# Kernel tuning notes

Measured on AMD Instinct MI355X. Metric: run time of the kernel, lower is better.

## Reference

```python
import jax, jax.numpy as jnp
import numpy as np

D_MODEL = 1024
NUM_HEADS = 16
HEAD_DIM = D_MODEL // NUM_HEADS  # 64


def setup_inputs() -> dict:
    key = jax.random.key(0)
    ks = jax.random.split(key, 9)
    s = 1.0 / np.sqrt(D_MODEL)
    return {
        "x": jax.random.normal(ks[0], (2, 2048, D_MODEL), dtype=jnp.float32),
        "Wq": jax.random.normal(ks[1], (D_MODEL, D_MODEL), dtype=jnp.float32) * s,
        "bq": jnp.zeros((D_MODEL,), dtype=jnp.float32),
        "Wk": jax.random.normal(ks[2], (D_MODEL, HEAD_DIM), dtype=jnp.float32) * s,
        "bk": jnp.zeros((HEAD_DIM,), dtype=jnp.float32),
        "Wv": jax.random.normal(ks[3], (D_MODEL, HEAD_DIM), dtype=jnp.float32) * s,
        "bv": jnp.zeros((HEAD_DIM,), dtype=jnp.float32),
        "Wo": jax.random.normal(ks[4], (D_MODEL, D_MODEL), dtype=jnp.float32) * s,
        "bo": jnp.zeros((D_MODEL,), dtype=jnp.float32),
    }


def reference(x, Wq, bq, Wk, bk, Wv, bv, Wo, bo):
    B, S, D = x.shape
    H, hd = NUM_HEADS, HEAD_DIM
    # Projections: Q has H heads, K/V a single shared head (MQA).
    Q = (x @ Wq + bq).reshape(B, S, H, hd).transpose(0, 2, 1, 3)  # [B,H,S,hd]
    K = x @ Wk + bk  # [B,S,hd]
    V = x @ Wv + bv  # [B,S,hd]
    # Shared-K/V attention: broadcast K across heads instead of expand().
    scores = jnp.einsum("bhqd,bkd->bhqk", Q, K) / np.sqrt(hd)  # [B,H,S,S]
    attn = jax.nn.softmax(scores, axis=-1)
    attended = jnp.einsum("bhqk,bkd->bhqd", attn, V)  # [B,H,S,hd]
    attended = attended.transpose(0, 2, 1, 3).reshape(B, S, D)
    return attended @ Wo + bo
```

## Files before the change

kernel.cpp:

```cpp
#include <hip/hip_runtime.h>
#include <hip/hip_bf16.h>

#define D_MODEL 1024
#define NHEADS  16
#define HD      64
#define BATCH   2
#define SEQ     2048
#define MROWS   4096
#define NQKV    1152
#define NSPLIT  2

typedef short  short4v __attribute__((ext_vector_type(4)));
typedef short  short8  __attribute__((ext_vector_type(8)));
typedef float  floatx4 __attribute__((ext_vector_type(4)));
typedef unsigned uint4v __attribute__((ext_vector_type(4)));

__device__ inline short f2bf(float f) {
  unsigned u = __builtin_bit_cast(unsigned, f);
  u = (u + 0x7FFF + ((u >> 16) & 1)) >> 16;
  return (short)u;
}

__device__ inline unsigned pack_trunc(float lo, float hi) {
  return __builtin_amdgcn_perm(__builtin_bit_cast(unsigned, hi),
                               __builtin_bit_cast(unsigned, lo), 0x07060302u);
}

__device__ inline void async_copy16(const short* g, short* l) {
  __builtin_amdgcn_global_load_lds(
      (const __attribute__((address_space(1))) unsigned int*)g,
      (__attribute__((address_space(3))) unsigned int*)l, 16, 0, 0);
}

__global__ __launch_bounds__(256)
void prep_kernel(const float* __restrict__ x,  const float* __restrict__ Wq,
                 const float* __restrict__ Wk, const float* __restrict__ Wv,
                 const float* __restrict__ Wo, const float* __restrict__ bq,
                 const float* __restrict__ bk, const float* __restrict__ bv,
                 short* __restrict__ xb, short* __restrict__ Wqkv_t,
                 short* __restrict__ Wo_t, float* __restrict__ bqkv) {
  const int id = blockIdx.x;
  const int t  = threadIdx.x;
  if (id < 544) {
    __shared__ short Ts[64 * 72];
    const float* src; short* dst; int N, off, tile;
    if (id < 256)      { src = Wq; dst = Wqkv_t; N = 1024; off = 0;    tile = id; }
    else if (id < 272) { src = Wk; dst = Wqkv_t; N = 64;   off = 1024; tile = id - 256; }
    else if (id < 288) { src = Wv; dst = Wqkv_t; N = 64;   off = 1088; tile = id - 272; }
    else               { src = Wo; dst = Wo_t;   N = 1024; off = 0;    tile = id - 288; }
    const int k0 = (N == 1024) ? (tile & 15) * 64 : tile * 64;
    const int n0 = (N == 1024) ? (tile >> 4) * 64 : 0;
    {
      const int r = t >> 2, c = (t & 3) * 16;
      const float* s = src + (size_t)(k0 + r) * N + n0 + c;
#pragma unroll
      for (int j = 0; j < 16; j += 4) {
        float4 v = *reinterpret_cast<const float4*>(s + j);
        Ts[r * 72 + c + j + 0] = f2bf(v.x); Ts[r * 72 + c + j + 1] = f2bf(v.y);
        Ts[r * 72 + c + j + 2] = f2bf(v.z); Ts[r * 72 + c + j + 3] = f2bf(v.w);
      }
    }
    __syncthreads();
    {
      const int n = t >> 2, kc = (t & 3) * 16;
      short8 o0, o1;
#pragma unroll
      for (int j = 0; j < 8; ++j) o0[j] = Ts[(kc + j) * 72 + n];
#pragma unroll
      for (int j = 0; j < 8; ++j) o1[j] = Ts[(kc + 8 + j) * 72 + n];
      short* d = dst + (size_t)(off + n0 + n) * 1024 + k0 + kc;
      *reinterpret_cast<short8*>(d)     = o0;
      *reinterpret_cast<short8*>(d + 8) = o1;
    }
  } else if (id < 549) {
    const int i = (id - 544) * 256 + t;
    if (i < 1024)      bqkv[i] = bq[i];
    else if (i < 1088) bqkv[i] = bk[i - 1024];
    else if (i < 1152) bqkv[i] = bv[i - 1088];
  } else {
    const int i = ((id - 549) * 256 + t) * 8;
    if (i < MROWS * D_MODEL) {
      float4 a = *reinterpret_cast<const float4*>(x + i);
      float4 b = *reinterpret_cast<const float4*>(x + i + 4);
      short8 o;
      o[0] = f2bf(a.x); o[1] = f2bf(a.y); o[2] = f2bf(a.z); o[3] = f2bf(a.w);
      o[4] = f2bf(b.x); o[5] = f2bf(b.y); o[6] = f2bf(b.z); o[7] = f2bf(b.w);
      *reinterpret_cast<short8*>(xb + i) = o;
    }
  }
}

template<bool OUT_BF16, int SCALE_N, bool VT_FUSE>
__global__ __launch_bounds__(256)
void gemm_mfma_bt(const short* __restrict__ A, const short* __restrict__ Bt,
                  const float* __restrict__ bias, void* __restrict__ Cout,
                  short* __restrict__ Vtg, int M, int N, int K) {
  __shared__ short As[2][128 * 64];
  __shared__ short Bs[2][64 * 64];
  const int t    = threadIdx.x;
  const int w    = t >> 6;
  const int lane = t & 63;
  const int quad = lane >> 4;
  const int l16  = lane & 15;
  const int bm   = blockIdx.x * 128;
  const int bn   = blockIdx.y * 64;
  const int wm   = (w >> 1) * 64;
  const int wn   = (w & 1) * 32;

  const int srow = t >> 3;
  const int cc   = ((t & 7) ^ (srow & 7)) * 8;
  const short* gA = A  + (size_t)(bm + srow) * K + cc;
  const short* gB = Bt + (size_t)(bn + srow) * K + cc;

  floatx4 acc[4][2];
#pragma unroll
  for (int i = 0; i < 4; ++i)
#pragma unroll
    for (int j = 0; j < 2; ++j) acc[i][j] = (floatx4){0.f, 0.f, 0.f, 0.f};

  const int xr = l16 & 7;

  async_copy16(gA, &As[0][t * 8]);
  async_copy16(gA + (size_t)32 * K, &As[0][t * 8 + 2048]);
  async_copy16(gA + (size_t)64 * K, &As[0][t * 8 + 4096]);
  async_copy16(gA + (size_t)96 * K, &As[0][t * 8 + 6144]);
  async_copy16(gB, &Bs[0][t * 8]);
  async_copy16(gB + (size_t)32 * K, &Bs[0][t * 8 + 2048]);

  int cur = 0;
  for (int k0 = 0; k0 < K; k0 += 64) {
    asm volatile("s_waitcnt vmcnt(0)" ::: "memory");
    __builtin_amdgcn_s_barrier();
    __builtin_amdgcn_sched_barrier(0);

    if (k0 + 64 < K) {
      const int nb = cur ^ 1;
      const int kn = k0 + 64;
      async_copy16(gA + kn, &As[nb][t * 8]);
      async_copy16(gA + (size_t)32 * K + kn, &As[nb][t * 8 + 2048]);
      async_copy16(gA + (size_t)64 * K + kn, &As[nb][t * 8 + 4096]);
      async_copy16(gA + (size_t)96 * K + kn, &As[nb][t * 8 + 6144]);
      async_copy16(gB + kn, &Bs[nb][t * 8]);
      async_copy16(gB + (size_t)32 * K + kn, &Bs[nb][t * 8 + 2048]);
    }
    __builtin_amdgcn_sched_barrier(0);

    const short* Ac = As[cur];
    const short* Bc = Bs[cur];
    short8 fa0[4], fa1[4], fb0[2], fb1[2];
#pragma unroll
    for (int mi = 0; mi < 4; ++mi) {
      const int row = wm + mi * 16 + l16;
      fa0[mi] = *reinterpret_cast<const short8*>(&Ac[row * 64 + (quad ^ xr) * 8]);
      fa1[mi] = *reinterpret_cast<const short8*>(&Ac[row * 64 + ((4 + quad) ^ xr) * 8]);
    }
#pragma unroll
    for (int ni = 0; ni < 2; ++ni) {
      const int row = wn + ni * 16 + l16;
      fb0[ni] = *reinterpret_cast<const short8*>(&Bc[row * 64 + (quad ^ xr) * 8]);
      fb1[ni] = *reinterpret_cast<const short8*>(&Bc[row * 64 + ((4 + quad) ^ xr) * 8]);
    }
#pragma unroll
    for (int mi = 0; mi < 4; ++mi)
#pragma unroll
      for (int ni = 0; ni < 2; ++ni) {
        acc[mi][ni] = __builtin_amdgcn_mfma_f32_16x16x32_bf16(fa0[mi], fb0[ni], acc[mi][ni], 0, 0, 0);
        acc[mi][ni] = __builtin_amdgcn_mfma_f32_16x16x32_bf16(fa1[mi], fb1[ni], acc[mi][ni], 0, 0, 0);
      }
    cur ^= 1;
  }

#pragma unroll
  for (int ni = 0; ni < 2; ++ni) {
    const int col = bn + wn + ni * 16 + l16;
    const float bs = bias[col];
    const float sc = (col < SCALE_N) ? 0.18033688f : 1.0f;
#pragma unroll
    for (int mi = 0; mi < 4; ++mi) {
      const int row = bm + wm + mi * 16 + quad * 4;
      short4v vt4;
#pragma unroll
      for (int r = 0; r < 4; ++r) {
        const float v = (acc[mi][ni][r] + bs) * sc;
        if (OUT_BF16) {
          const short bv16 = f2bf(v);
          ((short*)Cout)[(size_t)(row + r) * N + col] = bv16;
          if (VT_FUSE) vt4[r] = bv16;
        } else {
          ((float*)Cout)[(size_t)(row + r) * N + col] = v;
        }
      }
      if (VT_FUSE && col >= 1088) {
        const int d = col - 1088;
        const int b = row >> 11, s = row & 2047;
        *reinterpret_cast<short4v*>(&Vtg[(size_t)(b * 64 + d) * SEQ + s]) = vt4;
      }
    }
  }
}

__global__ __launch_bounds__(256, 3)
void mqa_flash_bf16(const short* __restrict__ QKV, const short* __restrict__ Vtg,
                    _Float16* __restrict__ Opart, float* __restrict__ lpart) {
  const int bh    = blockIdx.y;
  const int b     = bh >> 4;
  const int h     = bh & 15;
  const int s0    = blockIdx.x * 128;
  const int split = blockIdx.z;
  const int t     = threadIdx.x;
  const int w     = t >> 6;
  const int lane  = t & 63;
  const int quad  = lane >> 4;
  const int l16   = lane & 15;

  __shared__ short KVs[16384];

  short8 aq[2][2];
#pragma unroll
  for (int st = 0; st < 2; ++st) {
    const short* qrow = &QKV[(size_t)(b * SEQ + s0 + w * 32 + st * 16 + l16) * NQKV + h * HD];
    aq[st][0] = *reinterpret_cast<const short8*>(qrow + quad * 8);
    aq[st][1] = *reinterpret_cast<const short8*>(qrow + 32 + quad * 8);
  }

  floatx4 oacc[2][4];
  floatx4 lacc[2];
#pragma unroll
  for (int st = 0; st < 2; ++st) {
    lacc[st] = (floatx4){0.f, 0.f, 0.f, 0.f};
#pragma unroll
    for (int dg = 0; dg < 4; ++dg) oacc[st][dg] = (floatx4){0.f, 0.f, 0.f, 0.f};
  }

  short8 ones;
#pragma unroll
  for (int j = 0; j < 8; ++j) ones[j] = (short)0x3F80;

  const int srow  = t >> 3;
  const int cc    = ((t & 7) ^ (srow & 7)) * 8;
  const int krow  = ((srow >> 4) & 1) * 4 + ((srow >> 2) & 3) * 8 + (srow & 3);
  const int kbase = split * (SEQ / NSPLIT);
  const short* gK = QKV + (size_t)(b * SEQ + kbase + krow) * NQKV + 1024 + cc;
  const short* gV = Vtg + (size_t)(b * 64 + srow) * SEQ + kbase + cc;
  short* lK = KVs + w * 512;
  short* lV = KVs + 4096 + w * 512;

  const int xr = l16 & 7;

  async_copy16(gK, lK);
  async_copy16(gK + (size_t)32 * NQKV, lK + 2048);
  async_copy16(gV, lV);
  async_copy16(gV + (size_t)32 * SEQ, lV + 2048);
  gK += (size_t)64 * NQKV;
  gV += 64;

  const int NT = (SEQ / NSPLIT) / 64;
  int cur = 0;

  for (int it = 0; it < NT; ++it) {
    asm volatile("s_waitcnt vmcnt(0)" ::: "memory");
    __builtin_amdgcn_s_barrier();
    __builtin_amdgcn_sched_barrier(0);

    if (it + 1 < NT) {
      const int nb = (cur ^ 1) * 8192;
      async_copy16(gK, lK + nb);
      async_copy16(gK + (size_t)32 * NQKV, lK + nb + 2048);
      async_copy16(gV, lV + nb);
      async_copy16(gV + (size_t)32 * SEQ, lV + nb + 2048);
      gK += (size_t)64 * NQKV;
      gV += 64;
    }
    __builtin_amdgcn_sched_barrier(0);

    const short* Ks = KVs + cur * 8192;
    const short* Vt = Ks + 4096;

    short8 kb[4][2], vb[4][2];
#pragma unroll
    for (int kg = 0; kg < 4; ++kg) {
      kb[kg][0] = *reinterpret_cast<const short8*>(&Ks[(kg * 16 + l16) * 64 + (quad ^ xr) * 8]);
      kb[kg][1] = *reinterpret_cast<const short8*>(&Ks[(kg * 16 + l16) * 64 + ((4 + quad) ^ xr) * 8]);
    }
#pragma unroll
    for (int dg = 0; dg < 4; ++dg) {
      vb[dg][0] = *reinterpret_cast<const short8*>(&Vt[(dg * 16 + l16) * 64 + (quad ^ xr) * 8]);
      vb[dg][1] = *reinterpret_cast<const short8*>(&Vt[(dg * 16 + l16) * 64 + ((4 + quad) ^ xr) * 8]);
    }

#pragma unroll
    for (int st = 0; st < 2; ++st) {
      floatx4 s4[4];
#pragma unroll
      for (int kg = 0; kg < 4; ++kg) {
        s4[kg] = (floatx4){0.f, 0.f, 0.f, 0.f};
        s4[kg] = __builtin_amdgcn_mfma_f32_16x16x32_bf16(kb[kg][0], aq[st][0], s4[kg], 0, 0, 0);
        s4[kg] = __builtin_amdgcn_mfma_f32_16x16x32_bf16(kb[kg][1], aq[st][1], s4[kg], 0, 0, 0);
      }
      unsigned pk[8];
#pragma unroll
      for (int kg = 0; kg < 4; ++kg) {
        const float p0 = __builtin_exp2f(s4[kg][0]);
        const float p1 = __builtin_exp2f(s4[kg][1]);
        const float p2 = __builtin_exp2f(s4[kg][2]);
        const float p3 = __builtin_exp2f(s4[kg][3]);
        pk[kg * 2 + 0] = pack_trunc(p0, p1);
        pk[kg * 2 + 1] = pack_trunc(p2, p3);
      }
      const uint4v u0 = (uint4v){pk[0], pk[1], pk[2], pk[3]};
      const uint4v u1 = (uint4v){pk[4], pk[5], pk[6], pk[7]};
      const short8 ap0 = __builtin_bit_cast(short8, u0);
      const short8 ap1 = __builtin_bit_cast(short8, u1);

      __builtin_amdgcn_s_setprio(1);
      lacc[st] = __builtin_amdgcn_mfma_f32_16x16x32_bf16(ap0, ones, lacc[st], 0, 0, 0);
      lacc[st] = __builtin_amdgcn_mfma_f32_16x16x32_bf16(ap1, ones, lacc[st], 0, 0, 0);
#pragma unroll
      for (int dg = 0; dg < 4; ++dg) {
        oacc[st][dg] = __builtin_amdgcn_mfma_f32_16x16x32_bf16(ap0, vb[dg][0], oacc[st][dg], 0, 0, 0);
        oacc[st][dg] = __builtin_amdgcn_mfma_f32_16x16x32_bf16(ap1, vb[dg][1], oacc[st][dg], 0, 0, 0);
      }
      __builtin_amdgcn_s_setprio(0);
    }
    cur ^= 1;
  }

#pragma unroll
  for (int st = 0; st < 2; ++st) {
#pragma unroll
    for (int rg = 0; rg < 4; ++rg) {
      const int qg = s0 + w * 32 + st * 16 + quad * 4 + rg;
      _Float16* dst = Opart + ((size_t)(split * 32 + bh) * SEQ + qg) * 64 + l16;
#pragma unroll
      for (int dg = 0; dg < 4; ++dg) dst[dg * 16] = (_Float16)oacc[st][dg][rg];
      if (l16 == 0) lpart[(size_t)(split * 32 + bh) * SEQ + qg] = lacc[st][rg];
    }
  }
}

__global__ __launch_bounds__(256)
void combine_kernel(const _Float16* __restrict__ Opart, const float* __restrict__ lpart,
                    short* __restrict__ Att) {
  const int idx = blockIdx.x * 256 + threadIdx.x;
  const int r   = idx >> 3;
  const int d0  = (idx & 7) * 8;
  float l = 0.f;
  float o[8] = {0.f,0.f,0.f,0.f,0.f,0.f,0.f,0.f};
#pragma unroll
  for (int s = 0; s < NSPLIT; ++s) {
    const _Float16* op = Opart + ((size_t)(s * 32 * SEQ) + r) * 64 + d0;
    l += lpart[(size_t)s * 32 * SEQ + r];
#pragma unroll
    for (int j = 0; j < 8; ++j) o[j] += (float)op[j];
  }
  const float inv = 1.0f / l;
  short8 ov;
#pragma unroll
  for (int j = 0; j < 8; ++j) ov[j] = f2bf(o[j] * inv);
  const int bhh = r >> 11, q = r & 2047;
  const int bb = bhh >> 4, hh = bhh & 15;
  *reinterpret_cast<short8*>(&Att[(size_t)(bb * SEQ + q) * D_MODEL + hh * HD + d0]) = ov;
}

extern "C" void kernel_launch(void* const* d_in, const int* in_sizes, int n_in,
                              void* d_out, int out_size, void* d_ws, size_t ws_size,
                              hipStream_t stream) {
  const float* x  = (const float*)d_in[0];
  const float* Wq = (const float*)d_in[1];
  const float* bq = (const float*)d_in[2];
  const float* Wk = (const float*)d_in[3];
  const float* bk = (const float*)d_in[4];
  const float* Wv = (const float*)d_in[5];
  const float* bv = (const float*)d_in[6];
  const float* Wo = (const float*)d_in[7];
  const float* bo = (const float*)d_in[8];
  float* out = (float*)d_out;

  short* Wqkv_t = (short*)d_ws;
  short* Wo_t   = Wqkv_t + (size_t)NQKV * D_MODEL;
  short* xb     = Wo_t + (size_t)D_MODEL * D_MODEL;
  short* QKV    = xb + (size_t)MROWS * D_MODEL;
  short* Att    = QKV + (size_t)MROWS * NQKV;
  short* Vtg    = Att + (size_t)MROWS * D_MODEL;
  float* bqkv   = (float*)(Vtg + (size_t)BATCH * HD * SEQ);
  float* lpart  = bqkv + 1152;
  _Float16* Opart = (_Float16*)(lpart + (size_t)NSPLIT * 32 * SEQ);

  prep_kernel<<<2597, 256, 0, stream>>>(x, Wq, Wk, Wv, Wo, bq, bk, bv,
                                        xb, Wqkv_t, Wo_t, bqkv);

  gemm_mfma_bt<true, 1024, true><<<dim3(MROWS / 128, NQKV / 64), 256, 0, stream>>>(
      xb, Wqkv_t, bqkv, QKV, Vtg, MROWS, NQKV, D_MODEL);

  mqa_flash_bf16<<<dim3(SEQ / 128, BATCH * NHEADS, NSPLIT), 256, 0, stream>>>(
      QKV, Vtg, Opart, lpart);

  combine_kernel<<<2048, 256, 0, stream>>>(Opart, lpart, Att);

  gemm_mfma_bt<false, 0, false><<<dim3(MROWS / 128, D_MODEL / 64), 256, 0, stream>>>(
      Att, Wo_t, bo, out, nullptr, MROWS, D_MODEL, D_MODEL);
}
```

Measured before the change: 171.3 us.

## Drop split-K attention and combine kernel; use 128-key tiles with fused normalization

Removes the two-way key split and the separate combine kernel. Each flash block now walks the full sequence and normalizes by the row sum before writing bf16 straight into the attention buffer. K/V staging is widened to 128-key tiles, so LDS use doubles and the occupancy hint drops from 3 to 2 blocks. This avoids the fp16 partial-output round trip and one launch, at the cost of half as many blocks (512) in the grid and longer per-block loops.

```diff
diff --git a/kernel.cpp b/kernel.cpp
--- a/kernel.cpp
+++ b/kernel.cpp
@@ -8,7 +8,6 @@
 #define SEQ     2048
 #define MROWS   4096
 #define NQKV    1152
-#define NSPLIT  2
 
 typedef short  short4v __attribute__((ext_vector_type(4)));
 typedef short  short8  __attribute__((ext_vector_type(8)));
@@ -199,21 +198,20 @@
   }
 }
 
-__global__ __launch_bounds__(256, 3)
+__global__ __launch_bounds__(256, 2)
 void mqa_flash_bf16(const short* __restrict__ QKV, const short* __restrict__ Vtg,
-                    _Float16* __restrict__ Opart, float* __restrict__ lpart) {
-  const int bh    = blockIdx.y;
-  const int b     = bh >> 4;
-  const int h     = bh & 15;
-  const int s0    = blockIdx.x * 128;
-  const int split = blockIdx.z;
-  const int t     = threadIdx.x;
-  const int w     = t >> 6;
-  const int lane  = t & 63;
-  const int quad  = lane >> 4;
-  const int l16   = lane & 15;
-
-  __shared__ short KVs[16384];
+                    short* __restrict__ Att) {
+  const int bh   = blockIdx.y;
+  const int b    = bh >> 4;
+  const int h    = bh & 15;
+  const int s0   = blockIdx.x * 128;
+  const int t    = threadIdx.x;
+  const int w    = t >> 6;
+  const int lane = t & 63;
+  const int quad = lane >> 4;
+  const int l16  = lane & 15;
+
+  __shared__ short KVs[2][16384];
 
   short8 aq[2][2];
 #pragma unroll
@@ -236,25 +234,35 @@
 #pragma unroll
   for (int j = 0; j < 8; ++j) ones[j] = (short)0x3F80;
 
-  const int srow  = t >> 3;
-  const int cc    = ((t & 7) ^ (srow & 7)) * 8;
-  const int krow  = ((srow >> 4) & 1) * 4 + ((srow >> 2) & 3) * 8 + (srow & 3);
-  const int kbase = split * (SEQ / NSPLIT);
-  const short* gK = QKV + (size_t)(b * SEQ + kbase + krow) * NQKV + 1024 + cc;
-  const short* gV = Vtg + (size_t)(b * 64 + srow) * SEQ + kbase + cc;
-  short* lK = KVs + w * 512;
-  short* lV = KVs + 4096 + w * 512;
+  const int srow = t >> 3;
+  const int ccK  = ((t & 7) ^ (srow & 7)) * 8;
+  const int krow = ((srow >> 4) & 1) * 4 + ((srow >> 2) & 3) * 8 + (srow & 3);
+  const short* gK = QKV + (size_t)(b * SEQ + krow) * NQKV + 1024 + ccK;
+  const int vrow = t >> 4;
+  const int ccV  = ((t & 15) ^ (vrow & 7)) * 8;
+  const short* gV = Vtg + (size_t)(b * 64 + vrow) * SEQ + ccV;
 
   const int xr = l16 & 7;
 
-  async_copy16(gK, lK);
-  async_copy16(gK + (size_t)32 * NQKV, lK + 2048);
-  async_copy16(gV, lV);
-  async_copy16(gV + (size_t)32 * SEQ, lV + 2048);
-  gK += (size_t)64 * NQKV;
-  gV += 64;
-
-  const int NT = (SEQ / NSPLIT) / 64;
+#define STAGE(BUF)                                                     \
+  {                                                                    \
+    short* lK = KVs[BUF] + w * 512;                                    \
+    short* lV = KVs[BUF] + 8192 + w * 512;                             \
+    async_copy16(gK, lK);                                              \
+    async_copy16(gK + (size_t)32 * NQKV, lK + 2048);                   \
+    async_copy16(gK + (size_t)64 * NQKV, lK + 4096);                   \
+    async_copy16(gK + (size_t)96 * NQKV, lK + 6144);                   \
+    async_copy16(gV, lV);                                              \
+    async_copy16(gV + (size_t)16 * SEQ, lV + 2048);                    \
+    async_copy16(gV + (size_t)32 * SEQ, lV + 4096);                    \
+    async_copy16(gV + (size_t)48 * SEQ, lV + 6144);                    \
+    gK += (size_t)128 * NQKV;                                          \
+    gV += 128;                                                         \
+  }
+
+  STAGE(0)
+
+  const int NT = SEQ / 128;
   int cur = 0;
 
   for (int it = 0; it < NT; ++it) {
@@ -262,104 +270,78 @@
     __builtin_amdgcn_s_barrier();
     __builtin_amdgcn_sched_barrier(0);
 
-    if (it + 1 < NT) {
-      const int nb = (cur ^ 1) * 8192;
-      async_copy16(gK, lK + nb);
-      async_copy16(gK + (size_t)32 * NQKV, lK + nb + 2048);
-      async_copy16(gV, lV + nb);
-      async_copy16(gV + (size_t)32 * SEQ, lV + nb + 2048);
-      gK += (size_t)64 * NQKV;
-      gV += 64;
-    }
+    if (it + 1 < NT) STAGE(cur ^ 1)
     __builtin_amdgcn_sched_barrier(0);
 
-    const short* Ks = KVs + cur * 8192;
-    const short* Vt = Ks + 4096;
-
-    short8 kb[4][2], vb[4][2];
-#pragma unroll
-    for (int kg = 0; kg < 4; ++kg) {
-      kb[kg][0] = *reinterpret_cast<const short8*>(&Ks[(kg * 16 + l16) * 64 + (quad ^ xr) * 8]);
-      kb[kg][1] = *reinterpret_cast<const short8*>(&Ks[(kg * 16 + l16) * 64 + ((4 + quad) ^ xr) * 8]);
-    }
-#pragma unroll
-    for (int dg = 0; dg < 4; ++dg) {
-      vb[dg][0] = *reinterpret_cast<const short8*>(&Vt[(dg * 16 + l16) * 64 + (quad ^ xr) * 8]);
-      vb[dg][1] = *reinterpret_cast<const short8*>(&Vt[(dg * 16 + l16) * 64 + ((4 + quad) ^ xr) * 8]);
-    }
-
-#pragma unroll
-    for (int st = 0; st < 2; ++st) {
-      floatx4 s4[4];
+#pragma unroll
+    for (int half = 0; half < 2; ++half) {
+      const short* Ks = KVs[cur] + half * 4096;
+      const short* Vt = KVs[cur] + 8192;
+      const int vc = half * 8;
+
+      short8 kb[4][2], vb[4][2];
 #pragma unroll
       for (int kg = 0; kg < 4; ++kg) {
-        s4[kg] = (floatx4){0.f, 0.f, 0.f, 0.f};
-        s4[kg] = __builtin_amdgcn_mfma_f32_16x16x32_bf16(kb[kg][0], aq[st][0], s4[kg], 0, 0, 0);
-        s4[kg] = __builtin_amdgcn_mfma_f32_16x16x32_bf16(kb[kg][1], aq[st][1], s4[kg], 0, 0, 0);
-      }
-      unsigned pk[8];
-#pragma unroll
-      for (int kg = 0; kg < 4; ++kg) {
-        const float p0 = __builtin_exp2f(s4[kg][0]);
-        const float p1 = __builtin_exp2f(s4[kg][1]);
-        const float p2 = __builtin_exp2f(s4[kg][2]);
-        const float p3 = __builtin_exp2f(s4[kg][3]);
-        pk[kg * 2 + 0] = pack_trunc(p0, p1);
-        pk[kg * 2 + 1] = pack_trunc(p2, p3);
-      }
-      const uint4v u0 = (uint4v){pk[0], pk[1], pk[2], pk[3]};
-      const uint4v u1 = (uint4v){pk[4], pk[5], pk[6], pk[7]};
-      const short8 ap0 = __builtin_bit_cast(short8, u0);
-      const short8 ap1 = __builtin_bit_cast(short8, u1);
-
-      __builtin_amdgcn_s_setprio(1);
-      lacc[st] = __builtin_amdgcn_mfma_f32_16x16x32_bf16(ap0, ones, lacc[st], 0, 0, 0);
-      lacc[st] = __builtin_amdgcn_mfma_f32_16x16x32_bf16(ap1, ones, lacc[st], 0, 0, 0);
+        kb[kg][0] = *reinterpret_cast<const short8*>(&Ks[(kg * 16 + l16) * 64 + (quad ^ xr) * 8]);
+        kb[kg][1] = *reinterpret_cast<const short8*>(&Ks[(kg * 16 + l16) * 64 + ((4 + quad) ^ xr) * 8]);
+      }
 #pragma unroll
       for (int dg = 0; dg < 4; ++dg) {
-        oacc[st][dg] = __builtin_amdgcn_mfma_f32_16x16x32_bf16(ap0, vb[dg][0], oacc[st][dg], 0, 0, 0);
-        oacc[st][dg] = __builtin_amdgcn_mfma_f32_16x16x32_bf16(ap1, vb[dg][1], oacc[st][dg], 0, 0, 0);
-      }
-      __builtin_amdgcn_s_setprio(0);
+        vb[dg][0] = *reinterpret_cast<const short8*>(&Vt[(dg * 16 + l16) * 128 + (vc + (quad ^ xr)) * 8]);
+        vb[dg][1] = *reinterpret_cast<const short8*>(&Vt[(dg * 16 + l16) * 128 + (vc + ((4 + quad) ^ xr)) * 8]);
+      }
+
+#pragma unroll
+      for (int st = 0; st < 2; ++st) {
+        floatx4 s4[4];
+#pragma unroll
+        for (int kg = 0; kg < 4; ++kg) {
+          s4[kg] = (floatx4){0.f, 0.f, 0.f, 0.f};
+          s4[kg] = __builtin_amdgcn_mfma_f32_16x16x32_bf16(kb[kg][0], aq[st][0], s4[kg], 0, 0, 0);
+          s4[kg] = __builtin_amdgcn_mfma_f32_16x16x32_bf16(kb[kg][1], aq[st][1], s4[kg], 0, 0, 0);
+        }
+        unsigned pk[8];
+#pragma unroll
+        for (int kg = 0; kg < 4; ++kg) {
+          const float p0 = __builtin_exp2f(s4[kg][0]);
+          const float p1 = __builtin_exp2f(s4[kg][1]);
+          const float p2 = __builtin_exp2f(s4[kg][2]);
+          const float p3 = __builtin_exp2f(s4[kg][3]);
+          pk[kg * 2 + 0] = pack_trunc(p0, p1);
+          pk[kg * 2 + 1] = pack_trunc(p2, p3);
+        }
+        const uint4v u0 = (uint4v){pk[0], pk[1], pk[2], pk[3]};
+        const uint4v u1 = (uint4v){pk[4], pk[5], pk[6], pk[7]};
+        const short8 ap0 = __builtin_bit_cast(short8, u0);
+        const short8 ap1 = __builtin_bit_cast(short8, u1);
+
+        __builtin_amdgcn_s_setprio(1);
+        lacc[st] = __builtin_amdgcn_mfma_f32_16x16x32_bf16(ap0, ones, lacc[st], 0, 0, 0);
+        lacc[st] = __builtin_amdgcn_mfma_f32_16x16x32_bf16(ap1, ones, lacc[st], 0, 0, 0);
+#pragma unroll
+        for (int dg = 0; dg < 4; ++dg) {
+          oacc[st][dg] = __builtin_amdgcn_mfma_f32_16x16x32_bf16(ap0, vb[dg][0], oacc[st][dg], 0, 0, 0);
+          oacc[st][dg] = __builtin_amdgcn_mfma_f32_16x16x32_bf16(ap1, vb[dg][1], oacc[st][dg], 0, 0, 0);
+        }
+        __builtin_amdgcn_s_setprio(0);
+      }
     }
     cur ^= 1;
   }
-
+#undef STAGE
+
+  short* At = Att + (size_t)b * SEQ * D_MODEL + h * HD;
 #pragma unroll
   for (int st = 0; st < 2; ++st) {
 #pragma unroll
     for (int rg = 0; rg < 4; ++rg) {
-      const int qg = s0 + w * 32 + st * 16 + quad * 4 + rg;
-      _Float16* dst = Opart + ((size_t)(split * 32 + bh) * SEQ + qg) * 64 + l16;
-#pragma unroll
-      for (int dg = 0; dg < 4; ++dg) dst[dg * 16] = (_Float16)oacc[st][dg][rg];
-      if (l16 == 0) lpart[(size_t)(split * 32 + bh) * SEQ + qg] = lacc[st][rg];
-    }
-  }
-}
-
-__global__ __launch_bounds__(256)
-void combine_kernel(const _Float16* __restrict__ Opart, const float* __restrict__ lpart,
-                    short* __restrict__ Att) {
-  const int idx = blockIdx.x * 256 + threadIdx.x;
-  const int r   = idx >> 3;
-  const int d0  = (idx & 7) * 8;
-  float l = 0.f;
-  float o[8] = {0.f,0.f,0.f,0.f,0.f,0.f,0.f,0.f};
-#pragma unroll
-  for (int s = 0; s < NSPLIT; ++s) {
-    const _Float16* op = Opart + ((size_t)(s * 32 * SEQ) + r) * 64 + d0;
-    l += lpart[(size_t)s * 32 * SEQ + r];
-#pragma unroll
-    for (int j = 0; j < 8; ++j) o[j] += (float)op[j];
-  }
-  const float inv = 1.0f / l;
-  short8 ov;
-#pragma unroll
-  for (int j = 0; j < 8; ++j) ov[j] = f2bf(o[j] * inv);
-  const int bhh = r >> 11, q = r & 2047;
-  const int bb = bhh >> 4, hh = bhh & 15;
-  *reinterpret_cast<short8*>(&Att[(size_t)(bb * SEQ + q) * D_MODEL + hh * HD + d0]) = ov;
+      const int q = s0 + w * 32 + st * 16 + quad * 4 + rg;
+      const float inv = 1.0f / lacc[st][rg];
+      short* dst = At + (size_t)q * D_MODEL + l16;
+#pragma unroll
+      for (int dg = 0; dg < 4; ++dg) dst[dg * 16] = f2bf(oacc[st][dg][rg] * inv);
+    }
+  }
 }
 
 extern "C" void kernel_launch(void* const* d_in, const int* in_sizes, int n_in,
@@ -383,8 +365,6 @@
   short* Att    = QKV + (size_t)MROWS * NQKV;
   short* Vtg    = Att + (size_t)MROWS * D_MODEL;
   float* bqkv   = (float*)(Vtg + (size_t)BATCH * HD * SEQ);
-  float* lpart  = bqkv + 1152;
-  _Float16* Opart = (_Float16*)(lpart + (size_t)NSPLIT * 32 * SEQ);
 
   prep_kernel<<<2597, 256, 0, stream>>>(x, Wq, Wk, Wv, Wo, bq, bk, bv,
                                         xb, Wqkv_t, Wo_t, bqkv);
@@ -392,10 +372,8 @@
   gemm_mfma_bt<true, 1024, true><<<dim3(MROWS / 128, NQKV / 64), 256, 0, stream>>>(
       xb, Wqkv_t, bqkv, QKV, Vtg, MROWS, NQKV, D_MODEL);
 
-  mqa_flash_bf16<<<dim3(SEQ / 128, BATCH * NHEADS, NSPLIT), 256, 0, stream>>>(
-      QKV, Vtg, Opart, lpart);
-
-  combine_kernel<<<2048, 256, 0, stream>>>(Opart, lpart, Att);
+  mqa_flash_bf16<<<dim3(SEQ / 128, BATCH * NHEADS), 256, 0, stream>>>(
+      QKV, Vtg, Att);
 
   gemm_mfma_bt<false, 0, false><<<dim3(MROWS / 128, D_MODEL / 64), 256, 0, stream>>>(
       Att, Wo_t, bo, out, nullptr, MROWS, D_MODEL, D_MODEL);
```

Result: faster. 167.9 us (-2.0%).
